# Kernel tuning notes

Measured on AMD Instinct MI355X. Metric: run time of the kernel, lower is better.

The kernel has to match this reference:

```python
import jax, jax.numpy as jnp
import numpy as np

N_NODES = 207
N_EDGES = 1722
N_SLOTS = 288
RESOLUTION = 1
BATCH = 1024


def setup_inputs() -> dict:
    key = jax.random.key(0)
    ks = jax.random.split(key, 8)
    inputs = jax.random.normal(ks[0], (BATCH, 2, 12, N_NODES), dtype=jnp.float32)
    weight_react = jax.random.normal(ks[1], (N_SLOTS, N_EDGES), dtype=jnp.float32) / 10.0
    weight_diff = jax.random.normal(ks[2], (N_SLOTS, N_EDGES), dtype=jnp.float32) / 1000.0
    bias_reaction = jax.random.normal(ks[3], (N_SLOTS, N_NODES), dtype=jnp.float32) / 10.0
    bias_diffusion = jax.random.normal(ks[4], (N_SLOTS, N_NODES), dtype=jnp.float32) / 10.0
    weight_self_loop = jax.random.normal(ks[5], (N_SLOTS, N_NODES), dtype=jnp.float32) / 10.0
    ind = jax.random.randint(ks[6], (BATCH,), 0, N_SLOTS, dtype=jnp.int32)
    edge_index = jax.random.randint(ks[7], (2, N_EDGES), 0, N_NODES, dtype=jnp.int32)
    return {
        'inputs': inputs,
        'weight_react': weight_react,
        'weight_diff': weight_diff,
        'bias_reaction': bias_reaction,
        'bias_diffusion': bias_diffusion,
        'weight_self_loop': weight_self_loop,
        'ind': ind,
        'edge_index': edge_index,
    }


def _build_adjacency(edge_index, vals):
    """Symmetric dense adjacency per batch element.

    edge_index: [2, E] int; vals: [B, E] float.
    Returns A [B, N, N] with A[b, i, j] += v and A[b, j, i] += v (duplicates summed,
    matching torch.sparse_coo_tensor coalescing).
    """
    src = jnp.concatenate([edge_index[0], edge_index[1]])  # [2E]
    dst = jnp.concatenate([edge_index[1], edge_index[0]])  # [2E]
    v = jnp.concatenate([vals, vals], axis=1)              # [B, 2E]
    B = vals.shape[0]
    A = jnp.zeros((B, N_NODES, N_NODES), dtype=vals.dtype)
    return A.at[:, src, dst].add(v)


def reference(inputs, weight_react, weight_diff, bias_reaction, bias_diffusion,
              weight_self_loop, ind, edge_index):
    B = inputs.shape[0]
    # [B, d1, d2, N] -> [B, d1*d2, N] -> [B, N, L]
    x = inputs.reshape(B, -1, N_NODES).transpose(0, 2, 1)
    ii = ind // RESOLUTION  # time-of-day slot per sample, [B]

    A_r = _build_adjacency(edge_index, weight_react[ii])  # [B, N, N]
    A_d = _build_adjacency(edge_index, weight_diff[ii])   # [B, N, N]
    diag = jnp.arange(N_NODES)
    # torch sums dim 1 of [N, N] (column sums) and adds/subtracts diag of it
    d_r = A_r.sum(axis=1)  # [B, N]
    d_d = A_d.sum(axis=1)  # [B, N]
    R = A_r.at[:, diag, diag].add(d_r)   # diag(d) + A
    D = (-A_d).at[:, diag, diag].add(d_d)  # diag(d) - A

    # nconv: out[b, w, l] = sum_v x[b, v, l] * A[b, w, v]
    reaction = jnp.einsum('bvl,bwv->bwl', x, R) + bias_reaction[ii][:, :, None]
    diffusion = jnp.einsum('bvl,bwv->bwl', x, D) + bias_diffusion[ii][:, :, None]
    self_loop = weight_self_loop[ii][:, :, None] * x
    return jnp.tanh(reaction) + diffusion + x + self_loop  # [B, N, L]
```

## Files before the change

### kernel.cpp

```cpp
#include <hip/hip_runtime.h>

#define N_NODES 207
#define N_EDGES 1722
#define N_SLOTS 288
#define L_DIM 24
#define NPK 12
#define TOT_ENT (2 * N_EDGES)
#define THREADS 512

typedef float f32x2 __attribute__((ext_vector_type(2)));
typedef __fp16 h16x2 __attribute__((ext_vector_type(2)));

__device__ __forceinline__ unsigned pkrtz(float a, float b) {
    h16x2 h = __builtin_amdgcn_cvt_pkrtz(a, b);
    return __builtin_bit_cast(unsigned, h);
}
__device__ __forceinline__ f32x2 h2f(unsigned u) {
    h16x2 h = __builtin_bit_cast(h16x2, u);
    f32x2 r; r.x = (float)h.x; r.y = (float)h.y;
    return r;
}
__device__ __forceinline__ void fma_lo(unsigned& acc, unsigned wt, unsigned x) {
    asm("v_pk_fma_f16 %0, %1, %2, %0 op_sel:[0,0,0] op_sel_hi:[0,1,1]"
        : "+v"(acc) : "v"(wt), "v"(x));
}
__device__ __forceinline__ void fma_hi(unsigned& acc, unsigned wt, unsigned x) {
    asm("v_pk_fma_f16 %0, %1, %2, %0 op_sel:[1,0,0] op_sel_hi:[1,1,1]"
        : "+v"(acc) : "v"(wt), "v"(x));
}
__device__ __forceinline__ void addw(unsigned& sw, unsigned wt) {
    asm("v_pk_add_f16 %0, %1, %0" : "+v"(sw) : "v"(wt));
}
__device__ __forceinline__ float fast_tanhf(float x) {
    float e2 = __expf(2.0f * x);
    return 1.0f - 2.0f * __builtin_amdgcn_rcpf(e2 + 1.0f);
}

__global__ __launch_bounds__(THREADS, 4) void rdgcn_fused_kernel(
    const float* __restrict__ x_in,
    const float* __restrict__ w_react,
    const float* __restrict__ w_diff,
    const float* __restrict__ b_react,
    const float* __restrict__ b_diff,
    const float* __restrict__ w_self,
    const int* __restrict__ ind,
    const int* __restrict__ edge_index,
    float* __restrict__ out)
{
    __shared__ unsigned x_sh[2][N_NODES * NPK];
    __shared__ uint2    ewt_sh[2][TOT_ENT];

    const int tid  = threadIdx.x;
    const int h    = tid >> 8;
    const int htid = tid & 255;
    const int lane = tid & 63;
    const int wid  = tid >> 6;
    const int bA   = blockIdx.x * 2;
    const int b    = bA + h;
    const int sA   = ind[bA];
    const int sB   = ind[bA + 1];
    const int s    = h ? sB : sA;

    int ei[4], ej[4];
    int ne = 0;
    #pragma unroll
    for (int q = 0; q < 4; ++q) {
        const int e = tid + q * THREADS;
        if (e < N_EDGES) {
            ei[q] = edge_index[e];
            ej[q] = edge_index[N_EDGES + e];
            ne = q + 1;
        }
    }
    float wAr[4], wAd[4], wBr[4], wBd[4];
    {
        const float* wrgA = w_react + (size_t)sA * N_EDGES;
        const float* wdgA = w_diff  + (size_t)sA * N_EDGES;
        const float* wrgB = w_react + (size_t)sB * N_EDGES;
        const float* wdgB = w_diff  + (size_t)sB * N_EDGES;
        #pragma unroll
        for (int q = 0; q < 4; ++q) {
            const int e = tid + q * THREADS;
            if (e < N_EDGES) {
                wAr[q] = wrgA[e]; wAd[q] = wdgA[e];
                wBr[q] = wrgB[e]; wBd[q] = wdgB[e];
            }
        }
    }
    float r[L_DIM];
    if (htid < N_NODES) {
        const float* xg = x_in + (size_t)b * (L_DIM * N_NODES);
        #pragma unroll
        for (int l = 0; l < L_DIM; ++l) r[l] = xg[l * N_NODES + htid];
    }

    int* cnt_s  = (int*)x_sh;
    int* cur_s  = cnt_s + 208;
    int* off_s  = cur_s + 208;
    int* perm_s = off_s + 209;
    int* dcur_s = perm_s + 208;
    int* wsum_s = dcur_s + 64;

    if (tid < 208) cnt_s[tid] = 0;
    if (tid < 64)  dcur_s[tid] = 0;
    __syncthreads();

    for (int q = 0; q < ne; ++q) {
        atomicAdd(&cnt_s[ei[q]], 1);
        atomicAdd(&cnt_s[ej[q]], 1);
    }
    __syncthreads();

    const int deg  = (tid < N_NODES) ? cnt_s[tid] : 0;
    const int dcap = deg > 63 ? 63 : deg;
    int xs = deg;
    if (tid < 256) {
        #pragma unroll
        for (int sft = 1; sft < 64; sft <<= 1) {
            int t = __shfl_up(xs, sft, 64);
            if (lane >= sft) xs += t;
        }
        if (lane == 63) wsum_s[wid] = xs;
    }
    if (tid < N_NODES) atomicAdd(&dcur_s[dcap], 1);
    __syncthreads();

    int base = 0;
    if (tid < 256) { for (int i = 0; i < wid; ++i) base += wsum_s[i]; }
    const int excl = base + xs - deg;
    if (tid < N_NODES) { off_s[tid] = excl; cur_s[tid] = excl; }
    if (tid == 255)    off_s[N_NODES] = base + xs;

    if (tid < 64) {
        int hg = dcur_s[63 - tid];
        int ys = hg;
        #pragma unroll
        for (int sft = 1; sft < 64; sft <<= 1) {
            int t = __shfl_up(ys, sft, 64);
            if (lane >= sft) ys += t;
        }
        __syncthreads();
        dcur_s[63 - tid] = ys - hg;
    } else {
        __syncthreads();
    }
    __syncthreads();

    if (tid < N_NODES) {
        int p = atomicAdd(&dcur_s[dcap], 1);
        perm_s[p] = tid;
    }
    for (int q = 0; q < ne; ++q) {
        const unsigned wtA = pkrtz(wAr[q], wAd[q]);
        const unsigned wtB = pkrtz(wBr[q], wBd[q]);
        const int i = ei[q], j = ej[q];
        int pi = atomicAdd(&cur_s[i], 1);
        ewt_sh[0][pi] = make_uint2((unsigned)j, wtA);
        ewt_sh[1][pi] = make_uint2((unsigned)j, wtB);
        int pj = atomicAdd(&cur_s[j], 1);
        ewt_sh[0][pj] = make_uint2((unsigned)i, wtA);
        ewt_sh[1][pj] = make_uint2((unsigned)i, wtB);
    }
    __syncthreads();

    int w = 0, beg = 0, end = 0;
    if (htid < N_NODES) {
        w   = perm_s[htid];
        beg = off_s[w];
        end = off_s[w + 1];
    }
    __syncthreads();

    float br = 0.f, bd = 0.f, wsl = 0.f;
    if (htid < N_NODES) {
        br  = b_react[s * N_NODES + w];
        bd  = b_diff [s * N_NODES + w];
        wsl = w_self [s * N_NODES + w];
        unsigned p[NPK];
        #pragma unroll
        for (int i = 0; i < NPK; ++i) p[i] = pkrtz(r[2*i], r[2*i+1]);
        uint4* dst = reinterpret_cast<uint4*>(&x_sh[h][htid * NPK]);
        dst[0] = make_uint4(p[0], p[1], p[2],  p[3]);
        dst[1] = make_uint4(p[4], p[5], p[6],  p[7]);
        dst[2] = make_uint4(p[8], p[9], p[10], p[11]);
    }
    __syncthreads();

    if (htid >= N_NODES) return;

    unsigned accr[NPK] = {0,0,0,0,0,0,0,0,0,0,0,0};
    unsigned accd[NPK] = {0,0,0,0,0,0,0,0,0,0,0,0};
    unsigned sw = 0;

    const uint2*    ew  = ewt_sh[h];
    const unsigned* xsh = x_sh[h];
    for (int k = beg; k < end; ++k) {
        const uint2 q = ew[k];
        const unsigned wt = q.y;
        const uint4* xr = reinterpret_cast<const uint4*>(&xsh[q.x * NPK]);
        const uint4 qa = xr[0], qb = xr[1], qc = xr[2];
        addw(sw, wt);
        fma_lo(accr[0],  wt, qa.x);   fma_hi(accd[0],  wt, qa.x);
        fma_lo(accr[1],  wt, qa.y);   fma_hi(accd[1],  wt, qa.y);
        fma_lo(accr[2],  wt, qa.z);   fma_hi(accd[2],  wt, qa.z);
        fma_lo(accr[3],  wt, qa.w);   fma_hi(accd[3],  wt, qa.w);
        fma_lo(accr[4],  wt, qb.x);   fma_hi(accd[4],  wt, qb.x);
        fma_lo(accr[5],  wt, qb.y);   fma_hi(accd[5],  wt, qb.y);
        fma_lo(accr[6],  wt, qb.z);   fma_hi(accd[6],  wt, qb.z);
        fma_lo(accr[7],  wt, qb.w);   fma_hi(accd[7],  wt, qb.w);
        fma_lo(accr[8],  wt, qc.x);   fma_hi(accd[8],  wt, qc.x);
        fma_lo(accr[9],  wt, qc.y);   fma_hi(accd[9],  wt, qc.y);
        fma_lo(accr[10], wt, qc.z);   fma_hi(accd[10], wt, qc.z);
        fma_lo(accr[11], wt, qc.w);   fma_hi(accd[11], wt, qc.w);
    }

    const f32x2 sw2 = h2f(sw);
    const float swr = sw2.x, swd = sw2.y;

    const uint4* xw = reinterpret_cast<const uint4*>(&xsh[w * NPK]);
    const uint4 r0 = xw[0], r1 = xw[1], r2 = xw[2];
    const unsigned own[NPK] = { r0.x, r0.y, r0.z, r0.w,
                                r1.x, r1.y, r1.z, r1.w,
                                r2.x, r2.y, r2.z, r2.w };

    float o[L_DIM];
    #pragma unroll
    for (int i = 0; i < NPK; ++i) {
        const f32x2 xv = h2f(own[i]);
        const f32x2 ar = h2f(accr[i]);
        const f32x2 ad = h2f(accd[i]);
        {
            float re = fmaf(swr, xv.x,  ar.x) + br;
            float di = fmaf(swd, xv.x, -ad.x) + bd;
            o[2*i]   = fast_tanhf(re) + di + fmaf(xv.x, wsl, xv.x);
        }
        {
            float re = fmaf(swr, xv.y,  ar.y) + br;
            float di = fmaf(swd, xv.y, -ad.y) + bd;
            o[2*i+1] = fast_tanhf(re) + di + fmaf(xv.y, wsl, xv.y);
        }
    }
    float* op = out + (size_t)b * (N_NODES * L_DIM) + (size_t)w * L_DIM;
    reinterpret_cast<float4*>(op)[0] = make_float4(o[0],  o[1],  o[2],  o[3]);
    reinterpret_cast<float4*>(op)[1] = make_float4(o[4],  o[5],  o[6],  o[7]);
    reinterpret_cast<float4*>(op)[2] = make_float4(o[8],  o[9],  o[10], o[11]);
    reinterpret_cast<float4*>(op)[3] = make_float4(o[12], o[13], o[14], o[15]);
    reinterpret_cast<float4*>(op)[4] = make_float4(o[16], o[17], o[18], o[19]);
    reinterpret_cast<float4*>(op)[5] = make_float4(o[20], o[21], o[22], o[23]);
}

extern "C" void kernel_launch(void* const* d_in, const int* in_sizes, int n_in,
                              void* d_out, int out_size, void* d_ws, size_t ws_size,
                              hipStream_t stream) {
    const float* x_in     = (const float*)d_in[0];
    const float* w_react  = (const float*)d_in[1];
    const float* w_diff   = (const float*)d_in[2];
    const float* b_react  = (const float*)d_in[3];
    const float* b_diff   = (const float*)d_in[4];
    const float* w_self   = (const float*)d_in[5];
    const int*   ind      = (const int*)d_in[6];
    const int*   edge_idx = (const int*)d_in[7];
    float* out = (float*)d_out;

    const int B = in_sizes[6];
    rdgcn_fused_kernel<<<B / 2, THREADS, 0, stream>>>(x_in, w_react, w_diff,
                                                      b_react, b_diff, w_self,
                                                      ind, edge_idx, out);
}
```

Measured before the change: 24.68 us.

## Split heaviest rows' edge loops across idle helper threads

```diff
diff --git a/kernel.cpp b/kernel.cpp
--- a/kernel.cpp
+++ b/kernel.cpp
@@ -7,6 +7,7 @@
 #define NPK 12
 #define TOT_ENT (2 * N_EDGES)
 #define THREADS 512
+#define N_HELP 48
 
 typedef float f32x2 __attribute__((ext_vector_type(2)));
 typedef __fp16 h16x2 __attribute__((ext_vector_type(2)));
@@ -61,6 +62,9 @@
     const int sB   = ind[bA + 1];
     const int s    = h ? sB : sA;
 
+    const bool is_owner  = (htid < N_NODES);
+    const bool is_helper = (htid >= 208);
+
     int ei[4], ej[4];
     int ne = 0;
     #pragma unroll
@@ -88,7 +92,7 @@
         }
     }
     float r[L_DIM];
-    if (htid < N_NODES) {
+    if (is_owner) {
         const float* xg = x_in + (size_t)b * (L_DIM * N_NODES);
         #pragma unroll
         for (int l = 0; l < L_DIM; ++l) r[l] = xg[l * N_NODES + htid];
@@ -164,15 +168,22 @@
     __syncthreads();
 
     int w = 0, beg = 0, end = 0;
-    if (htid < N_NODES) {
+    if (is_owner) {
         w   = perm_s[htid];
         beg = off_s[w];
         end = off_s[w + 1];
+        if (htid < N_HELP) end = beg + ((end - beg + 1) >> 1);
+    } else if (is_helper) {
+        const int k = htid - 208;
+        const int wn = perm_s[k];
+        const int b0 = off_s[wn], e0 = off_s[wn + 1];
+        beg = b0 + ((e0 - b0 + 1) >> 1);
+        end = e0;
     }
     __syncthreads();
 
     float br = 0.f, bd = 0.f, wsl = 0.f;
-    if (htid < N_NODES) {
+    if (is_owner) {
         br  = b_react[s * N_NODES + w];
         bd  = b_diff [s * N_NODES + w];
         wsl = w_self [s * N_NODES + w];
@@ -185,8 +196,6 @@
         dst[2] = make_uint4(p[8], p[9], p[10], p[11]);
     }
     __syncthreads();
-
-    if (htid >= N_NODES) return;
 
     unsigned accr[NPK] = {0,0,0,0,0,0,0,0,0,0,0,0};
     unsigned accd[NPK] = {0,0,0,0,0,0,0,0,0,0,0,0};
@@ -214,14 +223,37 @@
         fma_lo(accr[11], wt, qc.w);   fma_hi(accd[11], wt, qc.w);
     }
 
+    unsigned own[NPK];
+    if (is_owner) {
+        const uint4* xw = reinterpret_cast<const uint4*>(&xsh[w * NPK]);
+        const uint4 r0 = xw[0], r1 = xw[1], r2 = xw[2];
+        own[0] = r0.x; own[1]  = r0.y; own[2]  = r0.z; own[3]  = r0.w;
+        own[4] = r1.x; own[5]  = r1.y; own[6]  = r1.z; own[7]  = r1.w;
+        own[8] = r2.x; own[9]  = r2.y; own[10] = r2.z; own[11] = r2.w;
+    }
+    __syncthreads();
+
+    unsigned* part = (unsigned*)x_sh;
+    if (is_helper) {
+        const int k = htid - 208;
+        unsigned* pp = part + (h * N_HELP + k) * 25;
+        #pragma unroll
+        for (int i = 0; i < NPK; ++i) { pp[i] = accr[i]; pp[NPK + i] = accd[i]; }
+        pp[24] = sw;
+    }
+    __syncthreads();
+
+    if (!is_owner) return;
+
+    if (htid < N_HELP) {
+        const unsigned* pp = part + (h * N_HELP + htid) * 25;
+        #pragma unroll
+        for (int i = 0; i < NPK; ++i) { addw(accr[i], pp[i]); addw(accd[i], pp[NPK + i]); }
+        addw(sw, pp[24]);
+    }
+
     const f32x2 sw2 = h2f(sw);
     const float swr = sw2.x, swd = sw2.y;
-
-    const uint4* xw = reinterpret_cast<const uint4*>(&xsh[w * NPK]);
-    const uint4 r0 = xw[0], r1 = xw[1], r2 = xw[2];
-    const unsigned own[NPK] = { r0.x, r0.y, r0.z, r0.w,
-                                r1.x, r1.y, r1.z, r1.w,
-                                r2.x, r2.y, r2.z, r2.w };
 
     float o[L_DIM];
     #pragma unroll
```

New measurement: 25.25 us. +2.3%, slower.
